# Optimization experiments

Hardware: AMD Instinct MI355X
Metric: run time of the kernel (lower is better)

## Reference

```python
import jax, jax.numpy as jnp
import numpy as np

CHANNELS = 512
NUM_HEADS = 8
GROUPS = 32
EPS = 1e-5


def setup_inputs() -> dict:
    key = jax.random.key(0)
    ks = jax.random.split(key, 7)
    C = CHANNELS
    x = jax.random.normal(ks[0], (8, C, 32, 32), dtype=jnp.float32)
    gn_weight = jnp.ones((C,), dtype=jnp.float32)
    gn_bias = jnp.zeros((C,), dtype=jnp.float32)
    # Conv1d(C, 3C, k=1) weights ~ N(0, 0.02) per init_weights
    qkv_w = 0.02 * jax.random.normal(ks[1], (3 * C, C), dtype=jnp.float32)
    qkv_b = 0.01 * jax.random.normal(ks[2], (3 * C,), dtype=jnp.float32)
    out_w = 0.02 * jax.random.normal(ks[3], (C, C), dtype=jnp.float32)
    out_b = 0.01 * jax.random.normal(ks[4], (C,), dtype=jnp.float32)
    return {"x": x, "gn_weight": gn_weight, "gn_bias": gn_bias,
            "qkv_w": qkv_w, "qkv_b": qkv_b, "out_w": out_w, "out_b": out_b}


def _forward(x, gn_weight, gn_bias, qkv_w, qkv_b, out_w, out_b):
    n, c, h, w = x.shape
    hw = h * w
    heads = NUM_HEADS
    cph = c // heads
    xs = x.reshape(n, c, hw)  # [N, C, HW]
    # GroupNorm over (channels-in-group, spatial)
    xg = xs.reshape(n, GROUPS, c // GROUPS, hw)
    mean = jnp.mean(xg, axis=(2, 3), keepdims=True)
    var = jnp.var(xg, axis=(2, 3), keepdims=True)
    xn = ((xg - mean) * jax.lax.rsqrt(var + EPS)).reshape(n, c, hw)
    xn = xn * gn_weight[None, :, None] + gn_bias[None, :, None]
    # 1x1 Conv1d QKV projection
    qkv = jnp.einsum('oc,ncl->nol', qkv_w, xn) + qkv_b[None, :, None]  # [N, 3C, HW]
    q, k, v = jnp.split(qkv, 3, axis=1)  # each [N, C, HW]
    q = q.reshape(n * heads, cph, hw)
    k = k.reshape(n * heads, cph, hw)
    v = v.reshape(n * heads, cph, hw)
    scale = 1.0 / np.sqrt(cph).astype(np.float32)
    scores = jnp.einsum('bci,bcj->bij', q, k) * scale  # [NH, HW, HW]
    attn = jax.nn.softmax(scores, axis=-1)
    weighted = jnp.einsum('bij,bcj->bic', attn, v)  # [NH, HW, cph]
    # Faithful to torch: reshape(n, -1, h, w) on [n*heads, hw, cph] layout
    weighted = weighted.reshape(n, c, h, w)
    out = jnp.einsum('oc,nchw->nohw', out_w, weighted) + out_b[None, :, None, None]
    return out


def reference(x, gn_weight, gn_bias, qkv_w, qkv_b, out_w, out_b):
    return _forward(x, gn_weight, gn_bias, qkv_w, qkv_b, out_w, out_b)
```

## Files before the change

### kernel.cpp

```cpp
#include <hip/hip_runtime.h>
#include <math.h>

#define N_    8
#define C_    512
#define HW_   1024
#define G_    32
#define CPG_  16
#define OC3_  1536
#define LOG2E 1.44269504f

typedef _Float16 f16;
typedef f16 f16x8 __attribute__((ext_vector_type(8)));
typedef f16 f16x4 __attribute__((ext_vector_type(4)));
typedef float f32x4 __attribute__((ext_vector_type(4)));

#define GLOAD_LDS16(g, l)                                                          \
    __builtin_amdgcn_global_load_lds(                                              \
        (const __attribute__((address_space(1))) unsigned int*)(const void*)(g),   \
        (__attribute__((address_space(3))) unsigned int*)(void*)(l), 16, 0, 0)

#define WAIT_VM0() __builtin_amdgcn_s_waitcnt(0x0F70)

__global__ __launch_bounds__(256) void pack_w(const float* __restrict__ qkv_w,
                                              const float* __restrict__ out_w,
                                              const float* __restrict__ qkv_b,
                                              f16* __restrict__ Wq,
                                              f16* __restrict__ Wo,
                                              float* __restrict__ qkv_bs) {
    const float QS = 0.125f * LOG2E;
    int idx = blockIdx.x * 256 + threadIdx.x;
    if (idx < 786432) {
        float v = qkv_w[idx];
        if (idx < 262144) v *= QS;
        Wq[idx] = (f16)v;
    } else if (idx < 786432 + 262144) {
        Wo[idx - 786432] = (f16)out_w[idx - 786432];
    } else if (idx < 786432 + 262144 + 1536) {
        int i = idx - 786432 - 262144;
        float v = qkv_b[i];
        if (i < 512) v *= QS;
        qkv_bs[i] = v;
    }
}

__global__ __launch_bounds__(256) void gn_pack(const float* __restrict__ x,
                                               const float* __restrict__ gw,
                                               const float* __restrict__ gb,
                                               f16* __restrict__ XT) {
    __shared__ float red1[4], red2[4];
    __shared__ float sm, srstd;
    int blk = blockIdx.x;
    int n = blk >> 5, g = blk & 31;
    size_t base = ((size_t)n * C_ + (size_t)g * CPG_) * HW_;
    const float4* xp4 = (const float4*)(x + base);
    float4 vals[16];
    float s1 = 0.f, s2 = 0.f;
#pragma unroll
    for (int r = 0; r < 16; r++) {
        float4 v = xp4[r * 256 + threadIdx.x];
        vals[r] = v;
        s1 += v.x + v.y + v.z + v.w;
        s2 += v.x * v.x + v.y * v.y + v.z * v.z + v.w * v.w;
    }
#pragma unroll
    for (int off = 32; off > 0; off >>= 1) {
        s1 += __shfl_down(s1, off, 64);
        s2 += __shfl_down(s2, off, 64);
    }
    int wave = threadIdx.x >> 6, lane = threadIdx.x & 63;
    if (lane == 0) { red1[wave] = s1; red2[wave] = s2; }
    __syncthreads();
    if (threadIdx.x == 0) {
        float t1 = red1[0] + red1[1] + red1[2] + red1[3];
        float t2 = red2[0] + red2[1] + red2[2] + red2[3];
        float mean = t1 * (1.f / 16384.f);
        float var  = t2 * (1.f / 16384.f) - mean * mean;
        sm = mean;
        srstd = rsqrtf(var + 1e-5f);
    }
    __syncthreads();
    float mean = sm, rstd = srstd;
    float av[16], bbv[16];
#pragma unroll
    for (int r = 0; r < 16; r++) {
        int c = g * CPG_ + r;
        av[r] = gw[c] * rstd;
        bbv[r] = gb[c] - mean * av[r];
    }
    f16x8 lo[4], hi[4];
#pragma unroll
    for (int r = 0; r < 16; r++) {
        float4 v = vals[r];
        float a = av[r], bb = bbv[r];
        f16 e0 = (f16)(v.x * a + bb), e1 = (f16)(v.y * a + bb);
        f16 e2 = (f16)(v.z * a + bb), e3 = (f16)(v.w * a + bb);
        if (r < 8) { lo[0][r] = e0; lo[1][r] = e1; lo[2][r] = e2; lo[3][r] = e3; }
        else { hi[0][r - 8] = e0; hi[1][r - 8] = e1; hi[2][r - 8] = e2; hi[3][r - 8] = e3; }
    }
    f16* xt = XT + ((size_t)n * HW_ + (size_t)threadIdx.x * 4) * C_ + g * CPG_;
#pragma unroll
    for (int comp = 0; comp < 4; comp++) {
        *(f16x8*)&xt[(size_t)comp * C_]     = lo[comp];
        *(f16x8*)&xt[(size_t)comp * C_ + 8] = hi[comp];
    }
}

template <bool FINAL>
__global__ __launch_bounds__(256, 4) void gemm_f16(const f16* __restrict__ A,
                                                   const f16* __restrict__ B,
                                                   const float* __restrict__ bias,
                                                   void* __restrict__ Yq,
                                                   f16* __restrict__ Yv) {
    __shared__ __align__(16) unsigned char smem[34816];
    f16* As = (f16*)smem;
    f16* Bs = (f16*)(smem + 16384);
    int tid = threadIdx.x, lane = tid & 63, w = tid >> 6;
    int m = lane & 15, quad = lane >> 4;
    int ow0 = (w & 1) * 64, lw0 = (w >> 1) * 64;
    int l0 = blockIdx.x * 128, o0 = blockIdx.y * 128, n = blockIdx.z;
    const f16* Bn = B + ((size_t)n * HW_ + l0) * 512;

    int rowT[4], sgT[4];
#pragma unroll
    for (int t = 0; t < 4; t++) {
        int q = (w * 4 + t) * 64 + lane;
        int row = q >> 3, seg = q & 7;
        rowT[t] = row;
        sgT[t] = seg ^ (row & 7);
    }
    f16x8 ra[4], rb[4];
#pragma unroll
    for (int t = 0; t < 4; t++) {
        ra[t] = *(const f16x8*)&A[(size_t)(o0 + rowT[t]) * 512 + sgT[t] * 8];
        rb[t] = *(const f16x8*)&Bn[(size_t)rowT[t] * 512 + sgT[t] * 8];
    }

    f32x4 acc[4][4];
#pragma unroll
    for (int i = 0; i < 4; i++)
#pragma unroll
        for (int j = 0; j < 4; j++)
#pragma unroll
            for (int r = 0; r < 4; r++) acc[i][j][r] = 0.f;

    for (int c0 = 0; c0 < 512; c0 += 64) {
        __syncthreads();
#pragma unroll
        for (int t = 0; t < 4; t++) {
            int q = (w * 4 + t) * 64 + lane;
            *(f16x8*)&As[q * 8] = ra[t];
            *(f16x8*)&Bs[q * 8] = rb[t];
        }
        __syncthreads();
        if (c0 + 64 < 512) {
#pragma unroll
            for (int t = 0; t < 4; t++) {
                ra[t] = *(const f16x8*)&A[(size_t)(o0 + rowT[t]) * 512 + c0 + 64 + sgT[t] * 8];
                rb[t] = *(const f16x8*)&Bn[(size_t)rowT[t] * 512 + c0 + 64 + sgT[t] * 8];
            }
        }
#pragma unroll
        for (int ks = 0; ks < 2; ks++) {
            f16x8 af[4], bf[4];
#pragma unroll
            for (int ib = 0; ib < 4; ib++) {
                int row = ow0 + ib * 16 + m;
                int seg = (ks * 4 + quad) ^ (row & 7);
                af[ib] = *(const f16x8*)&As[row * 64 + seg * 8];
            }
#pragma unroll
            for (int jb = 0; jb < 4; jb++) {
                int row = lw0 + jb * 16 + m;
                int seg = (ks * 4 + quad) ^ (row & 7);
                bf[jb] = *(const f16x8*)&Bs[row * 64 + seg * 8];
            }
#pragma unroll
            for (int ib = 0; ib < 4; ib++)
#pragma unroll
                for (int jb = 0; jb < 4; jb++)
                    acc[ib][jb] = __builtin_amdgcn_mfma_f32_16x16x32_f16(
                        af[ib], bf[jb], acc[ib][jb], 0, 0, 0);
        }
    }

    float bv[4][4];
#pragma unroll
    for (int ib = 0; ib < 4; ib++)
#pragma unroll
        for (int r = 0; r < 4; r++)
            bv[ib][r] = bias[o0 + ow0 + ib * 16 + quad * 4 + r];

    if (FINAL) {
        float* on = (float*)Yq + (size_t)n * C_ * HW_;
#pragma unroll
        for (int ib = 0; ib < 4; ib++)
#pragma unroll
            for (int jb = 0; jb < 4; jb++)
#pragma unroll
                for (int r = 0; r < 4; r++)
                    on[(size_t)(o0 + ow0 + ib * 16 + quad * 4 + r) * HW_ +
                       l0 + lw0 + jb * 16 + m] = acc[ib][jb][r] + bv[ib][r];
    } else if (o0 >= 1024) {
        f16* vn = Yv + (size_t)n * C_ * HW_;
#pragma unroll
        for (int ib = 0; ib < 4; ib++)
#pragma unroll
            for (int jb = 0; jb < 4; jb++)
#pragma unroll
                for (int r = 0; r < 4; r++)
                    vn[(size_t)(o0 - 1024 + ow0 + ib * 16 + quad * 4 + r) * HW_ +
                       l0 + lw0 + jb * 16 + m] = (f16)(acc[ib][jb][r] + bv[ib][r]);
    } else {
        __syncthreads();
        f16* T = (f16*)smem;
#pragma unroll
        for (int ib = 0; ib < 4; ib++)
#pragma unroll
            for (int jb = 0; jb < 4; jb++) {
                f16x4 h;
#pragma unroll
                for (int r = 0; r < 4; r++) h[r] = (f16)(acc[ib][jb][r] + bv[ib][r]);
                int l = lw0 + jb * 16 + m;
                int oo = ow0 + ib * 16 + quad * 4;
                *(f16x4*)&T[l * 136 + oo] = h;
            }
        __syncthreads();
        f16* qn = (f16*)Yq + (size_t)n * HW_ * 1024;
#pragma unroll
        for (int rep = 0; rep < 8; rep++) {
            int idx = rep * 256 + tid;
            int l = idx >> 4, seg = idx & 15;
            f16x8 v = *(const f16x8*)&T[l * 136 + seg * 8];
            *(f16x8*)&qn[(size_t)(l0 + l) * 1024 + o0 + seg * 8] = v;
        }
    }
}

__global__ __launch_bounds__(256, 4) void attn_f16(const f16* __restrict__ qkvT,
                                                   const f16* __restrict__ vbuf,
                                                   f16* __restrict__ w2T) {
    __shared__ __align__(16) unsigned char smem[40960];
    f16* Kb0  = (f16*)smem;
    f16* Vb0  = (f16*)(smem + 16384);
    f16* Ps   = (f16*)(smem + 32768);
    f16* LDSo = (f16*)smem;

    int tid = threadIdx.x;
    int lane = tid & 63, wave = tid >> 6;
    int m = lane & 15, quad = lane >> 4;
    int iw = wave * 16;
    int bh = blockIdx.y, n = bh >> 3, head = bh & 7;
    int i0 = blockIdx.x * 64;
    const f16* qb = qkvT + (size_t)n * HW_ * 1024 + head * 64;
    const f16* kb = qb + 512;
    const f16* vb = vbuf + (size_t)n * C_ * HW_ + (size_t)head * 64 * HW_;

    f16x8 aq0 = *(const f16x8*)&qb[(size_t)(i0 + iw + m) * 1024 + quad * 8];
    f16x8 aq1 = *(const f16x8*)&qb[(size_t)(i0 + iw + m) * 1024 + 32 + quad * 8];

#pragma unroll
    for (int it = 0; it < 2; it++) {
        int chunk = it * 256 + tid;
        int row = chunk >> 3, seg = chunk & 7;
        int segg = seg ^ (row & 7);
        GLOAD_LDS16(kb + (size_t)row * 1024 + segg * 8,
                    Kb0 + ((size_t)it * 256 + wave * 64) * 8);
        GLOAD_LDS16(vb + (size_t)row * HW_ + segg * 8,
                    Vb0 + ((size_t)it * 256 + wave * 64) * 8);
    }

    f32x4 oacc[4];
#pragma unroll
    for (int cb = 0; cb < 4; cb++)
#pragma unroll
        for (int r = 0; r < 4; r++) oacc[cb][r] = 0.f;
    float lpart[4] = {0.f, 0.f, 0.f, 0.f};

    for (int jt = 0; jt < 16; jt++) {
        int p = jt & 1;
        const f16* Kp = Kb0 + p * 4096;
        const f16* Vp = Vb0 + p * 4096;
        WAIT_VM0();
        __syncthreads();
        if (jt < 15) {
            int j0n = (jt + 1) * 64;
            f16* Kn = Kb0 + (1 - p) * 4096;
            f16* Vn = Vb0 + (1 - p) * 4096;
#pragma unroll
            for (int it = 0; it < 2; it++) {
                int chunk = it * 256 + tid;
                int row = chunk >> 3, seg = chunk & 7;
                int segg = seg ^ (row & 7);
                GLOAD_LDS16(kb + (size_t)(j0n + row) * 1024 + segg * 8,
                            Kn + ((size_t)it * 256 + wave * 64) * 8);
                GLOAD_LDS16(vb + (size_t)row * HW_ + j0n + segg * 8,
                            Vn + ((size_t)it * 256 + wave * 64) * 8);
            }
        }

        f32x4 sacc[4];
#pragma unroll
        for (int jb = 0; jb < 4; jb++)
#pragma unroll
            for (int r = 0; r < 4; r++) sacc[jb][r] = 0.f;
#pragma unroll
        for (int jb = 0; jb < 4; jb++) {
            int row = jb * 16 + m;
            f16x8 b0 = *(const f16x8*)&Kp[row * 64 + ((quad ^ (row & 7)) * 8)];
            sacc[jb] = __builtin_amdgcn_mfma_f32_16x16x32_f16(aq0, b0, sacc[jb], 0, 0, 0);
        }
#pragma unroll
        for (int jb = 0; jb < 4; jb++) {
            int row = jb * 16 + m;
            f16x8 b1 = *(const f16x8*)&Kp[row * 64 + (((4 + quad) ^ (row & 7)) * 8)];
            sacc[jb] = __builtin_amdgcn_mfma_f32_16x16x32_f16(aq1, b1, sacc[jb], 0, 0, 0);
        }

#pragma unroll
        for (int r = 0; r < 4; r++) {
            int prow = iw + quad * 4 + r;
            int rw = prow & 7;
#pragma unroll
            for (int jb = 0; jb < 4; jb++) {
                float pv = exp2f(sacc[jb][r]);
                f16 pb = (f16)pv;
                int lseg = jb * 2 + (m >> 3);
                Ps[prow * 64 + ((lseg ^ rw) * 8) + (m & 7)] = pb;
                lpart[r] += (float)pb;
            }
        }
        __syncthreads();

#pragma unroll
        for (int ks = 0; ks < 2; ks++) {
            int prow = iw + m;
            f16x8 ap = *(const f16x8*)&Ps[prow * 64 + (((ks * 4 + quad) ^ (prow & 7)) * 8)];
#pragma unroll
            for (int cb = 0; cb < 4; cb++) {
                int vrow = cb * 16 + m;
                f16x8 bvv = *(const f16x8*)&Vp[vrow * 64 +
                                               (((ks * 4 + quad) ^ (vrow & 7)) * 8)];
                oacc[cb] = __builtin_amdgcn_mfma_f32_16x16x32_f16(ap, bvv, oacc[cb], 0, 0, 0);
            }
        }
    }

    float linv[4];
#pragma unroll
    for (int r = 0; r < 4; r++) {
        float ls = lpart[r];
#pragma unroll
        for (int off = 1; off < 16; off <<= 1)
            ls += __shfl_xor(ls, off, 64);
        linv[r] = 1.f / ls;
    }
    WAIT_VM0();
    __syncthreads();
#pragma unroll
    for (int cb = 0; cb < 4; cb++)
#pragma unroll
        for (int r = 0; r < 4; r++) {
            int s = (quad * 4 + r) * 64 + cb * 16 + m;
            LDSo[s * 4 + wave] = (f16)(oacc[cb][r] * linv[r]);
        }
    __syncthreads();
    f16* w2n = w2T + (size_t)n * HW_ * 512;
    int chbase = head * 64 + (i0 >> 4);
#pragma unroll
    for (int it = 0; it < 4; it++) {
        int s = it * 256 + tid;
        *(f16x4*)&w2n[(size_t)s * 512 + chbase] = *(const f16x4*)&LDSo[s * 4];
    }
}

extern "C" void kernel_launch(void* const* d_in, const int* in_sizes, int n_in,
                              void* d_out, int out_size, void* d_ws, size_t ws_size,
                              hipStream_t stream) {
    (void)in_sizes; (void)n_in; (void)out_size; (void)ws_size;
    const float* x     = (const float*)d_in[0];
    const float* gw    = (const float*)d_in[1];
    const float* gb    = (const float*)d_in[2];
    const float* qkv_w = (const float*)d_in[3];
    const float* qkv_b = (const float*)d_in[4];
    const float* out_w = (const float*)d_in[5];
    const float* out_b = (const float*)d_in[6];
    float* out = (float*)d_out;
    char* ws = (char*)d_ws;

    const size_t MB = 1024 * 1024;
    f16*   qkvT   = (f16*)ws;
    f16*   XT     = (f16*)(ws + 16 * MB);
    f16*   vbuf   = (f16*)(ws + 24 * MB);
    f16*   w2T    = (f16*)(ws + 32 * MB);
    f16*   Wq     = (f16*)(ws + 40 * MB);
    f16*   Wo     = (f16*)(ws + 42 * MB);
    float* qkv_bs = (float*)(ws + 43 * MB);

    pack_w<<<dim3(4103), 256, 0, stream>>>(qkv_w, out_w, qkv_b, Wq, Wo, qkv_bs);
    gn_pack<<<dim3(N_ * G_), 256, 0, stream>>>(x, gw, gb, XT);
    gemm_f16<false><<<dim3(8, 12, N_), 256, 0, stream>>>(Wq, XT, qkv_bs, (void*)qkvT, vbuf);
    attn_f16<<<dim3(16, 64), 256, 0, stream>>>(qkvT, vbuf, w2T);
    gemm_f16<true><<<dim3(8, 4, N_), 256, 0, stream>>>(Wo, w2T, out_b, (void*)out, nullptr);
}
```

Baseline: 172.1 us.

## Merge prep kernels, use direct global-to-LDS loads in GEMM, remap attention blocks per XCD

Merges the weight-packing and GroupNorm kernels into one launch, which removes a kernel launch and lets the two run concurrently. The GEMM drops register-staged prefetching in favour of global_load_lds straight into shared memory, waiting on vmcnt before each tile. Because the next tile is no longer prefetched, load latency is no longer overlapped with compute. The attention grid is flattened and remapped so that blocks sharing a batch-head land on the same XCD, aiming for better L2 reuse of K/V.

```diff
diff --git a/kernel.cpp b/kernel.cpp
--- a/kernel.cpp
+++ b/kernel.cpp
@@ -21,34 +21,35 @@
 
 #define WAIT_VM0() __builtin_amdgcn_s_waitcnt(0x0F70)
 
-__global__ __launch_bounds__(256) void pack_w(const float* __restrict__ qkv_w,
-                                              const float* __restrict__ out_w,
-                                              const float* __restrict__ qkv_b,
-                                              f16* __restrict__ Wq,
-                                              f16* __restrict__ Wo,
-                                              float* __restrict__ qkv_bs) {
-    const float QS = 0.125f * LOG2E;
-    int idx = blockIdx.x * 256 + threadIdx.x;
-    if (idx < 786432) {
-        float v = qkv_w[idx];
-        if (idx < 262144) v *= QS;
-        Wq[idx] = (f16)v;
-    } else if (idx < 786432 + 262144) {
-        Wo[idx - 786432] = (f16)out_w[idx - 786432];
-    } else if (idx < 786432 + 262144 + 1536) {
-        int i = idx - 786432 - 262144;
-        float v = qkv_b[i];
-        if (i < 512) v *= QS;
-        qkv_bs[i] = v;
-    }
-}
-
-__global__ __launch_bounds__(256) void gn_pack(const float* __restrict__ x,
-                                               const float* __restrict__ gw,
-                                               const float* __restrict__ gb,
-                                               f16* __restrict__ XT) {
+__global__ __launch_bounds__(256) void prep(const float* __restrict__ x,
+                                            const float* __restrict__ gw,
+                                            const float* __restrict__ gb,
+                                            f16* __restrict__ XT,
+                                            const float* __restrict__ qkv_w,
+                                            const float* __restrict__ out_w,
+                                            const float* __restrict__ qkv_b,
+                                            f16* __restrict__ Wq,
+                                            f16* __restrict__ Wo,
+                                            float* __restrict__ qkv_bs) {
     __shared__ float red1[4], red2[4];
     __shared__ float sm, srstd;
+    if (blockIdx.x >= 256) {
+        const float QS = 0.125f * LOG2E;
+        int idx = (blockIdx.x - 256) * 256 + threadIdx.x;
+        if (idx < 786432) {
+            float v = qkv_w[idx];
+            if (idx < 262144) v *= QS;
+            Wq[idx] = (f16)v;
+        } else if (idx < 786432 + 262144) {
+            Wo[idx - 786432] = (f16)out_w[idx - 786432];
+        } else if (idx < 786432 + 262144 + 1536) {
+            int i = idx - 786432 - 262144;
+            float v = qkv_b[i];
+            if (i < 512) v *= QS;
+            qkv_bs[i] = v;
+        }
+        return;
+    }
     int blk = blockIdx.x;
     int n = blk >> 5, g = blk & 31;
     size_t base = ((size_t)n * C_ + (size_t)g * CPG_) * HW_;
@@ -128,12 +129,6 @@
         rowT[t] = row;
         sgT[t] = seg ^ (row & 7);
     }
-    f16x8 ra[4], rb[4];
-#pragma unroll
-    for (int t = 0; t < 4; t++) {
-        ra[t] = *(const f16x8*)&A[(size_t)(o0 + rowT[t]) * 512 + sgT[t] * 8];
-        rb[t] = *(const f16x8*)&Bn[(size_t)rowT[t] * 512 + sgT[t] * 8];
-    }
 
     f32x4 acc[4][4];
 #pragma unroll
@@ -147,18 +142,13 @@
         __syncthreads();
 #pragma unroll
         for (int t = 0; t < 4; t++) {
-            int q = (w * 4 + t) * 64 + lane;
-            *(f16x8*)&As[q * 8] = ra[t];
-            *(f16x8*)&Bs[q * 8] = rb[t];
-        }
-        __syncthreads();
-        if (c0 + 64 < 512) {
-#pragma unroll
-            for (int t = 0; t < 4; t++) {
-                ra[t] = *(const f16x8*)&A[(size_t)(o0 + rowT[t]) * 512 + c0 + 64 + sgT[t] * 8];
-                rb[t] = *(const f16x8*)&Bn[(size_t)rowT[t] * 512 + c0 + 64 + sgT[t] * 8];
-            }
-        }
+            GLOAD_LDS16(A + (size_t)(o0 + rowT[t]) * 512 + c0 + sgT[t] * 8,
+                        As + (size_t)(w * 4 + t) * 512);
+            GLOAD_LDS16(Bn + (size_t)rowT[t] * 512 + c0 + sgT[t] * 8,
+                        Bs + (size_t)(w * 4 + t) * 512);
+        }
+        WAIT_VM0();
+        __syncthreads();
 #pragma unroll
         for (int ks = 0; ks < 2; ks++) {
             f16x8 af[4], bf[4];
@@ -249,8 +239,11 @@
     int lane = tid & 63, wave = tid >> 6;
     int m = lane & 15, quad = lane >> 4;
     int iw = wave * 16;
-    int bh = blockIdx.y, n = bh >> 3, head = bh & 7;
-    int i0 = blockIdx.x * 64;
+    int flat = blockIdx.x;
+    int xcd = flat & 7, slot = flat >> 3;
+    int itile = slot >> 3, bh = (slot & 7) * 8 + xcd;
+    int n = bh >> 3, head = bh & 7;
+    int i0 = itile * 64;
     const f16* qb = qkvT + (size_t)n * HW_ * 1024 + head * 64;
     const f16* kb = qb + 512;
     const f16* vb = vbuf + (size_t)n * C_ * HW_ + (size_t)head * 64 * HW_;
@@ -396,9 +389,9 @@
     f16*   Wo     = (f16*)(ws + 42 * MB);
     float* qkv_bs = (float*)(ws + 43 * MB);
 
-    pack_w<<<dim3(4103), 256, 0, stream>>>(qkv_w, out_w, qkv_b, Wq, Wo, qkv_bs);
-    gn_pack<<<dim3(N_ * G_), 256, 0, stream>>>(x, gw, gb, XT);
+    prep<<<dim3(256 + 4103), 256, 0, stream>>>(x, gw, gb, XT,
+                                               qkv_w, out_w, qkv_b, Wq, Wo, qkv_bs);
     gemm_f16<false><<<dim3(8, 12, N_), 256, 0, stream>>>(Wq, XT, qkv_bs, (void*)qkvT, vbuf);
-    attn_f16<<<dim3(16, 64), 256, 0, stream>>>(qkvT, vbuf, w2T);
+    attn_f16<<<dim3(1024), 256, 0, stream>>>(qkvT, vbuf, w2T);
     gemm_f16<true><<<dim3(8, 4, N_), 256, 0, stream>>>(Wo, w2T, out_b, (void*)out, nullptr);
 }
```

After: 159.1 us. 7.6% less time.
